# Kernel tuning notes

Hardware: AMD Instinct MI355X
Metric: run time of the kernel (lower is better)

## Reference

```python
import jax, jax.numpy as jnp
import numpy as np

B, S, H, NH = 2, 2048, 1024, 16
HD = H // NH


def setup_inputs() -> dict:
    key = jax.random.key(0)
    ks = jax.random.split(key, 12)
    query = jax.random.normal(ks[0], (B, S, H), dtype=jnp.float32)
    key_t = jax.random.normal(ks[1], (B, S, H), dtype=jnp.float32)
    value = jax.random.normal(ks[2], (B, S, H), dtype=jnp.float32)
    kpm = jax.random.randint(ks[3], (B, S), 0, 2).astype(bool)
    kpm = kpm.at[:, 0].set(False)  # guarantee at least one unmasked key per row
    bias = jax.random.normal(ks[4], (1, NH, S, S), dtype=jnp.float32)
    init = 0.02
    q_w = jax.random.normal(ks[5], (H, H), dtype=jnp.float32) * init
    k_w = jax.random.normal(ks[6], (H, H), dtype=jnp.float32) * init
    v_w = jax.random.normal(ks[7], (H, H), dtype=jnp.float32) * init
    o_w = jax.random.normal(ks[8], (H, H), dtype=jnp.float32) * init
    q_b = jnp.zeros((H,), jnp.float32)
    k_b = jnp.zeros((H,), jnp.float32)
    v_b = jnp.zeros((H,), jnp.float32)
    o_b = jnp.zeros((H,), jnp.float32)
    return {"query": query, "key": key_t, "value": value,
            "key_padding_mask": kpm, "bias": bias,
            "q_w": q_w, "q_b": q_b, "k_w": k_w, "k_b": k_b,
            "v_w": v_w, "v_b": v_b, "o_w": o_w, "o_b": o_b}


def _shape(x):
    # [B, S, H] -> [B, NH, S, HD]
    b, s, _ = x.shape
    return x.reshape(b, s, NH, HD).transpose(0, 2, 1, 3)


def reference(query, key, value, key_padding_mask, bias,
              q_w, q_b, k_w, k_b, v_w, v_b, o_w, o_b):
    scale = HD ** -0.5
    q = _shape(query @ q_w.T + q_b)
    k = _shape(key @ k_w.T + k_b)
    v = _shape(value @ v_w.T + v_b)
    attn = jnp.einsum('bhqd,bhkd->bhqk', q, k) * scale + bias
    mask = key_padding_mask[:, None, None, :]  # [B,1,1,S]
    attn = jnp.where(mask, -jnp.inf, attn)
    probs = jax.nn.softmax(attn, axis=-1)
    # safe-softmax: zero masked entries and renormalize with clamped denom
    probs = jnp.where(mask, 0.0, probs)
    denom = jnp.maximum(probs.sum(axis=-1, keepdims=True), 1e-6)
    probs = probs / denom
    ctx = jnp.einsum('bhqk,bhkd->bhqd', probs, v)
    ctx = ctx.transpose(0, 2, 1, 3).reshape(query.shape[0], query.shape[1], H)
    return ctx @ o_w.T + o_b
```

## Files before the change

### kernel.cpp

```cpp
#include <hip/hip_runtime.h>
#include <math.h>

#define Ss  2048
#define Hh  1024

typedef unsigned short u16;
typedef __attribute__((ext_vector_type(8))) short short8;
typedef __attribute__((ext_vector_type(4))) float fx4;

__device__ __forceinline__ u16 f2bf(float f) {
  unsigned int u = __float_as_uint(f);
  u = (u + 0x7fffu + ((u >> 16) & 1u)) >> 16;
  return (u16)u;
}

__device__ __forceinline__ void gld_lds16(const u16* g, u16* l) {
  __builtin_amdgcn_global_load_lds(
      (const __attribute__((address_space(1))) unsigned int*)(const unsigned int*)g,
      (__attribute__((address_space(3))) unsigned int*)(unsigned int*)l, 16, 0, 0);
}

#define MFMA16(a,b,c) __builtin_amdgcn_mfma_f32_16x16x32_bf16((a),(b),(c),0,0,0)

__global__ __launch_bounds__(256) void cast3(const float* __restrict__ a,
    const float* __restrict__ b, const float* __restrict__ c,
    u16* __restrict__ oa, u16* __restrict__ ob, u16* __restrict__ oc) {
  const int z = blockIdx.z;
  const float* in = z == 0 ? a : (z == 1 ? b : c);
  u16* out = z == 0 ? oa : (z == 1 ? ob : oc);
  const int i = (blockIdx.x * 256 + threadIdx.x) * 4;
  const float4 v = *(const float4*)(in + i);
  ushort4 r; r.x = f2bf(v.x); r.y = f2bf(v.y); r.z = f2bf(v.z); r.w = f2bf(v.w);
  *(ushort4*)(out + i) = r;
}

__global__ __launch_bounds__(256) void cast4(const float* __restrict__ a,
    const float* __restrict__ b, const float* __restrict__ c, const float* __restrict__ d,
    u16* __restrict__ oa, u16* __restrict__ ob, u16* __restrict__ oc, u16* __restrict__ od) {
  const int z = blockIdx.z;
  const float* in = z == 0 ? a : (z == 1 ? b : (z == 2 ? c : d));
  u16* out = z == 0 ? oa : (z == 1 ? ob : (z == 2 ? oc : od));
  const int i = (blockIdx.x * 256 + threadIdx.x) * 4;
  const float4 v = *(const float4*)(in + i);
  ushort4 r; r.x = f2bf(v.x); r.y = f2bf(v.y); r.z = f2bf(v.z); r.w = f2bf(v.w);
  *(ushort4*)(out + i) = r;
}

__global__ __launch_bounds__(256) void build_maskadd(const int* __restrict__ kpm,
                                                     float* __restrict__ ma) {
  const int i = blockIdx.x * 256 + threadIdx.x;
  ma[i] = kpm[i] ? -1.0e30f : 0.0f;
}

template <int MODE>
__device__ __forceinline__ void gemm_core(const u16* __restrict__ A,
    const u16* __restrict__ W, const float* __restrict__ bias,
    void* __restrict__ out, float scale) {
  __shared__ __align__(16) u16 As[2][4096];
  __shared__ __align__(16) u16 Bs[2][4096];
  const int tid = threadIdx.x;
  const int w = tid >> 6, lane = tid & 63, ln = lane & 15, quad = lane >> 4;
  const int i0 = blockIdx.y * 128, j0 = blockIdx.x * 128;
  const int wr = (w & 1) * 64, wc = (w >> 1) * 64;
  fx4 acc[4][4] = {};
  const int L0 = w * 64 + lane, L1 = L0 + 256;
  const u16* sa0 = A + (size_t)(i0 + (L0 & 127)) * 1024 + (L0 >> 7) * 8;
  const u16* sa1 = A + (size_t)(i0 + (L1 & 127)) * 1024 + (L1 >> 7) * 8;
  const u16* sb0 = W + (size_t)(j0 + (L0 & 127)) * 1024 + (L0 >> 7) * 8;
  const u16* sb1 = W + (size_t)(j0 + (L1 & 127)) * 1024 + (L1 >> 7) * 8;
  const int d0 = (w * 64) * 8, d1 = (256 + w * 64) * 8;

  gld_lds16(sa0, &As[0][d0]); gld_lds16(sa1, &As[0][d1]);
  gld_lds16(sb0, &Bs[0][d0]); gld_lds16(sb1, &Bs[0][d1]);
  __syncthreads();

  for (int k0 = 0; k0 < 1024; k0 += 32) {
    const int cur = (k0 >> 5) & 1;
    if (k0 + 32 < 1024) {
      const int nb = cur ^ 1;
      gld_lds16(sa0 + k0 + 32, &As[nb][d0]); gld_lds16(sa1 + k0 + 32, &As[nb][d1]);
      gld_lds16(sb0 + k0 + 32, &Bs[nb][d0]); gld_lds16(sb1 + k0 + 32, &Bs[nb][d1]);
    }
    short8 a[4], b[4];
#pragma unroll
    for (int t = 0; t < 4; ++t) {
      a[t] = *(const short8*)&As[cur][(quad * 128 + wr + t * 16 + ln) * 8];
      b[t] = *(const short8*)&Bs[cur][(quad * 128 + wc + t * 16 + ln) * 8];
    }
#pragma unroll
    for (int mt = 0; mt < 4; ++mt)
#pragma unroll
      for (int nt = 0; nt < 4; ++nt)
        acc[mt][nt] = MFMA16(a[mt], b[nt], acc[mt][nt]);
    __syncthreads();
  }
#pragma unroll
  for (int nt = 0; nt < 4; ++nt) {
    const int col = j0 + wc + nt * 16 + ln;
    const float bv = bias[col];
#pragma unroll
    for (int mt = 0; mt < 4; ++mt)
#pragma unroll
      for (int r = 0; r < 4; ++r) {
        const int row = i0 + wr + mt * 16 + quad * 4 + r;
        const float val = (acc[mt][nt][r] + bv) * scale;
        if (MODE == 1) {
          const int bb = row >> 11, s = row & 2047, h = col >> 6, d = col & 63;
          ((u16*)out)[((size_t)(bb * 16 + h) * 2048 + s) * 64 + d] = f2bf(val);
        } else {
          ((float*)out)[(size_t)row * 1024 + col] = val;
        }
      }
  }
}

__global__ __launch_bounds__(256) void gemm_qkv(
    const u16* xq, const u16* xk, const u16* xv,
    const u16* wq, const u16* wk, const u16* wv,
    const float* bq, const float* bk, const float* bv,
    u16* q, u16* k, u16* v) {
  const int z = blockIdx.z;
  const u16* A = z == 0 ? xq : (z == 1 ? xk : xv);
  const u16* W = z == 0 ? wq : (z == 1 ? wk : wv);
  const float* bb = z == 0 ? bq : (z == 1 ? bk : bv);
  u16* o = z == 0 ? q : (z == 1 ? k : v);
  const float sc = z == 0 ? 0.125f : 1.0f;
  gemm_core<1>(A, W, bb, o, sc);
}

__global__ __launch_bounds__(256) void gemm_o(const u16* ctx, const u16* wo,
                                              const float* ob, float* out) {
  gemm_core<0>(ctx, wo, ob, out, 1.0f);
}

__global__ __launch_bounds__(256) void transpose_v(const u16* __restrict__ v,
                                                   u16* __restrict__ vt) {
  __shared__ u16 T[64][72];
  const int tid = threadIdx.x;
  const int bh = blockIdx.y, s0 = blockIdx.x * 64;
#pragma unroll
  for (int i = 0; i < 2; ++i) {
    const int L = i * 256 + tid, key = L >> 3, dc = L & 7;
    const uint4 val = *(const uint4*)&v[((size_t)bh * 2048 + s0 + key) * 64 + dc * 8];
    *(uint4*)&T[key][dc * 8] = val;
  }
  __syncthreads();
#pragma unroll
  for (int i = 0; i < 2; ++i) {
    const int L = i * 256 + tid, d = L >> 3, kc = L & 7;
    u16 tmp[8];
#pragma unroll
    for (int j = 0; j < 8; ++j) tmp[j] = T[kc * 8 + j][d];
    *(uint4*)&vt[((size_t)bh * 64 + d) * 2048 + s0 + kc * 8] = *(const uint4*)tmp;
  }
}

__global__ __launch_bounds__(256) void attn(const u16* __restrict__ Qb,
    const u16* __restrict__ Kb, const u16* __restrict__ VT,
    const float* __restrict__ bias, const float* __restrict__ maskadd,
    u16* __restrict__ ctx) {
  __shared__ __align__(16) u16 Ks[2][4096];
  __shared__ __align__(16) u16 Vs[2][4096];
  __shared__ __align__(16) u16 Ps[4096];
  const int tid = threadIdx.x;
  const int w = tid >> 6, lane = tid & 63, ln = lane & 15, quad = lane >> 4;
  const int q0 = blockIdx.x * 64;
  const int hb = blockIdx.y, h = hb >> 1, b = hb & 1, bh = b * 16 + h;
  const int wr = w * 16;

  short8 qf[2];
#pragma unroll
  for (int ks = 0; ks < 2; ++ks)
    qf[ks] = *(const short8*)&Qb[((size_t)bh * 2048 + q0 + wr + ln) * 64 +
                                 ks * 32 + quad * 8];
  float mi[4], li[4];
  fx4 O[4] = {};
#pragma unroll
  for (int r = 0; r < 4; ++r) { mi[r] = -3.0e38f; li[r] = 0.f; }

  const int L0 = w * 64 + lane, L1 = L0 + 256;
  const u16* sk0 = Kb + ((size_t)bh * 2048 + (L0 & 63)) * 64 + (L0 >> 6) * 8;
  const u16* sk1 = Kb + ((size_t)bh * 2048 + (L1 & 63)) * 64 + (L1 >> 6) * 8;
  const u16* sv0 = VT + ((size_t)bh * 64 + (L0 & 63)) * 2048 + (L0 >> 6) * 8;
  const u16* sv1 = VT + ((size_t)bh * 64 + (L1 & 63)) * 2048 + (L1 >> 6) * 8;
  const int d0 = (w * 64) * 8, d1 = (256 + w * 64) * 8;

  const float* bq = bias + (size_t)h * Ss * Ss;

  gld_lds16(sk0, &Ks[0][d0]); gld_lds16(sk1, &Ks[0][d1]);
  gld_lds16(sv0, &Vs[0][d0]); gld_lds16(sv1, &Vs[0][d1]);
  float bcur[4][4], macur[4];
#pragma unroll
  for (int r = 0; r < 4; ++r) {
    const int qg = q0 + wr + quad * 4 + r;
#pragma unroll
    for (int nt = 0; nt < 4; ++nt)
      bcur[nt][r] = bq[(size_t)qg * Ss + nt * 16 + ln];
  }
#pragma unroll
  for (int nt = 0; nt < 4; ++nt) macur[nt] = maskadd[b * Ss + nt * 16 + ln];
  __syncthreads();

  for (int kt = 0; kt < Ss; kt += 64) {
    const int cur = (kt >> 6) & 1;
    if (kt + 64 < Ss) {
      const int nb = cur ^ 1;
      gld_lds16(sk0 + (size_t)(kt + 64) * 64, &Ks[nb][d0]);
      gld_lds16(sk1 + (size_t)(kt + 64) * 64, &Ks[nb][d1]);
      gld_lds16(sv0 + kt + 64, &Vs[nb][d0]);
      gld_lds16(sv1 + kt + 64, &Vs[nb][d1]);
    }
    const int kn = (kt + 64 < Ss) ? kt + 64 : kt;
    float bnxt[4][4], manxt[4];
#pragma unroll
    for (int r = 0; r < 4; ++r) {
      const int qg = q0 + wr + quad * 4 + r;
#pragma unroll
      for (int nt = 0; nt < 4; ++nt)
        bnxt[nt][r] = bq[(size_t)qg * Ss + kn + nt * 16 + ln];
    }
#pragma unroll
    for (int nt = 0; nt < 4; ++nt) manxt[nt] = maskadd[b * Ss + kn + nt * 16 + ln];

    fx4 S[4] = {};
#pragma unroll
    for (int ks = 0; ks < 2; ++ks)
#pragma unroll
      for (int nt = 0; nt < 4; ++nt) {
        const short8 kf = *(const short8*)&Ks[cur][((ks * 4 + quad) * 64 + nt * 16 + ln) * 8];
        S[nt] = MFMA16(qf[ks], kf, S[nt]);
      }

    float alpha[4];
#pragma unroll
    for (int r = 0; r < 4; ++r) {
      const float s0 = S[0][r] + bcur[0][r] + macur[0];
      const float s1 = S[1][r] + bcur[1][r] + macur[1];
      const float s2 = S[2][r] + bcur[2][r] + macur[2];
      const float s3 = S[3][r] + bcur[3][r] + macur[3];
      float mx = fmaxf(fmaxf(s0, s1), fmaxf(s2, s3));
      mx = fmaxf(mx, __shfl_xor(mx, 1)); mx = fmaxf(mx, __shfl_xor(mx, 2));
      mx = fmaxf(mx, __shfl_xor(mx, 4)); mx = fmaxf(mx, __shfl_xor(mx, 8));
      const float mn = fmaxf(mi[r], mx);
      const float a = __expf(mi[r] - mn);
      const float p0 = __expf(s0 - mn), p1 = __expf(s1 - mn);
      const float p2 = __expf(s2 - mn), p3 = __expf(s3 - mn);
      float rs = p0 + p1 + p2 + p3;
      rs += __shfl_xor(rs, 1); rs += __shfl_xor(rs, 2);
      rs += __shfl_xor(rs, 4); rs += __shfl_xor(rs, 8);
      li[r] = li[r] * a + rs;
      mi[r] = mn; alpha[r] = a;
      const int q = wr + quad * 4 + r;
      const int kcb = ln >> 3, jj = ln & 7;
      Ps[((kcb    ) * 64 + q) * 8 + jj] = f2bf(p0);
      Ps[((kcb + 2) * 64 + q) * 8 + jj] = f2bf(p1);
      Ps[((kcb + 4) * 64 + q) * 8 + jj] = f2bf(p2);
      Ps[((kcb + 6) * 64 + q) * 8 + jj] = f2bf(p3);
    }

#pragma unroll
    for (int nt = 0; nt < 4; ++nt)
#pragma unroll
      for (int r = 0; r < 4; ++r) O[nt][r] *= alpha[r];

#pragma unroll
    for (int ks = 0; ks < 2; ++ks) {
      const short8 pf = *(const short8*)&Ps[((ks * 4 + quad) * 64 + wr + ln) * 8];
#pragma unroll
      for (int nt = 0; nt < 4; ++nt) {
        const short8 vf = *(const short8*)&Vs[cur][((ks * 4 + quad) * 64 + nt * 16 + ln) * 8];
        O[nt] = MFMA16(pf, vf, O[nt]);
      }
    }

#pragma unroll
    for (int r = 0; r < 4; ++r) {
      macur[r] = manxt[r];
#pragma unroll
      for (int nt = 0; nt < 4; ++nt) bcur[nt][r] = bnxt[nt][r];
    }
    __syncthreads();
  }

#pragma unroll
  for (int r = 0; r < 4; ++r) {
    const float inv = 1.0f / fmaxf(li[r], 1e-6f);
    const int qg = q0 + wr + quad * 4 + r;
#pragma unroll
    for (int nt = 0; nt < 4; ++nt)
      ctx[((size_t)(b * Ss + qg)) * 1024 + h * 64 + nt * 16 + ln] =
          f2bf(O[nt][r] * inv);
  }
}

extern "C" void kernel_launch(void* const* d_in, const int* in_sizes, int n_in,
                              void* d_out, int out_size, void* d_ws, size_t ws_size,
                              hipStream_t stream) {
  const float* query = (const float*)d_in[0];
  const float* key   = (const float*)d_in[1];
  const float* value = (const float*)d_in[2];
  const int*   kpm   = (const int*)d_in[3];
  const float* bias  = (const float*)d_in[4];
  const float* q_w   = (const float*)d_in[5];
  const float* q_b   = (const float*)d_in[6];
  const float* k_w   = (const float*)d_in[7];
  const float* k_b   = (const float*)d_in[8];
  const float* v_w   = (const float*)d_in[9];
  const float* v_b   = (const float*)d_in[10];
  const float* o_w   = (const float*)d_in[11];
  const float* o_b   = (const float*)d_in[12];
  float* out = (float*)d_out;

  char* ws = (char*)d_ws;
  const size_t MB = 1024 * 1024;
  u16* xq = (u16*)(ws + 0 * MB);
  u16* xk = (u16*)(ws + 8 * MB);
  u16* xv = (u16*)(ws + 16 * MB);
  u16* wq = (u16*)(ws + 24 * MB);
  u16* wk = (u16*)(ws + 26 * MB);
  u16* wv = (u16*)(ws + 28 * MB);
  u16* wo = (u16*)(ws + 30 * MB);
  u16* qb = (u16*)(ws + 32 * MB);
  u16* kb = (u16*)(ws + 40 * MB);
  u16* vb = (u16*)(ws + 48 * MB);
  u16* cx = (u16*)(ws + 56 * MB);
  u16* vt = (u16*)(ws + 0 * MB);
  float* ma = (float*)(ws + 8 * MB);

  cast3<<<dim3(4096, 1, 3), 256, 0, stream>>>(query, key, value, xq, xk, xv);
  cast4<<<dim3(1024, 1, 4), 256, 0, stream>>>(q_w, k_w, v_w, o_w, wq, wk, wv, wo);
  gemm_qkv<<<dim3(8, 32, 3), 256, 0, stream>>>(xq, xk, xv, wq, wk, wv,
                                               q_b, k_b, v_b, qb, kb, vb);
  transpose_v<<<dim3(32, 32), 256, 0, stream>>>(vb, vt);
  build_maskadd<<<dim3(16), 256, 0, stream>>>(kpm, ma);
  attn<<<dim3(32, 32), 256, 0, stream>>>(qb, kb, vt, bias, ma, cx);
  gemm_o<<<dim3(8, 32), 256, 0, stream>>>(cx, wo, o_b, out);
}
```

Baseline: 611.2 us.

## Transpose QK^T MFMA so each lane owns a query row; lazy rescale softmax

Swaps the MFMA operands so S is computed transposed and each lane holds one query row's scores. Row max and row sum then need only two cross-lane shuffles instead of four per row. Bias and mask are loaded as float4 vectors and pre-summed. The online-softmax rescale of O is skipped unless some row's max grows by more than 8, and P is packed to bf16 with v_cvt_pk_bf16_f32 and stored as 8-byte LDS writes. This cuts shuffle, exp and scalar-store overhead in the inner loop. In exchange, skipping the rescale lets exp values reach e^8 before being stored as bf16, and O gains extra per-row shuffles when a rescale does happen.

```diff
diff --git a/kernel.cpp b/kernel.cpp
--- a/kernel.cpp
+++ b/kernel.cpp
@@ -173,10 +173,8 @@
   for (int ks = 0; ks < 2; ++ks)
     qf[ks] = *(const short8*)&Qb[((size_t)bh * 2048 + q0 + wr + ln) * 64 +
                                  ks * 32 + quad * 8];
-  float mi[4], li[4];
+  float mi = -3.0e38f, li = 0.f;
   fx4 O[4] = {};
-#pragma unroll
-  for (int r = 0; r < 4; ++r) { mi[r] = -3.0e38f; li[r] = 0.f; }
 
   const int L0 = w * 64 + lane, L1 = L0 + 256;
   const u16* sk0 = Kb + ((size_t)bh * 2048 + (L0 & 63)) * 64 + (L0 >> 6) * 8;
@@ -185,20 +183,19 @@
   const u16* sv1 = VT + ((size_t)bh * 64 + (L1 & 63)) * 2048 + (L1 >> 6) * 8;
   const int d0 = (w * 64) * 8, d1 = (256 + w * 64) * 8;
 
-  const float* bq = bias + (size_t)h * Ss * Ss;
+  const float* bp = bias + (size_t)h * Ss * Ss + (size_t)(q0 + wr + ln) * Ss + quad * 4;
+  const float* mp = maskadd + b * Ss + quad * 4;
 
   gld_lds16(sk0, &Ks[0][d0]); gld_lds16(sk1, &Ks[0][d1]);
   gld_lds16(sv0, &Vs[0][d0]); gld_lds16(sv1, &Vs[0][d1]);
-  float bcur[4][4], macur[4];
-#pragma unroll
-  for (int r = 0; r < 4; ++r) {
-    const int qg = q0 + wr + quad * 4 + r;
-#pragma unroll
-    for (int nt = 0; nt < 4; ++nt)
-      bcur[nt][r] = bq[(size_t)qg * Ss + nt * 16 + ln];
-  }
-#pragma unroll
-  for (int nt = 0; nt < 4; ++nt) macur[nt] = maskadd[b * Ss + nt * 16 + ln];
+  fx4 bm[4];
+#pragma unroll
+  for (int nt = 0; nt < 4; ++nt) {
+    const float4 bv = *(const float4*)(bp + nt * 16);
+    const float4 mv = *(const float4*)(mp + nt * 16);
+    bm[nt][0] = bv.x + mv.x; bm[nt][1] = bv.y + mv.y;
+    bm[nt][2] = bv.z + mv.z; bm[nt][3] = bv.w + mv.w;
+  }
   __syncthreads();
 
   for (int kt = 0; kt < Ss; kt += 64) {
@@ -211,16 +208,14 @@
       gld_lds16(sv1 + kt + 64, &Vs[nb][d1]);
     }
     const int kn = (kt + 64 < Ss) ? kt + 64 : kt;
-    float bnxt[4][4], manxt[4];
-#pragma unroll
-    for (int r = 0; r < 4; ++r) {
-      const int qg = q0 + wr + quad * 4 + r;
-#pragma unroll
-      for (int nt = 0; nt < 4; ++nt)
-        bnxt[nt][r] = bq[(size_t)qg * Ss + kn + nt * 16 + ln];
-    }
-#pragma unroll
-    for (int nt = 0; nt < 4; ++nt) manxt[nt] = maskadd[b * Ss + kn + nt * 16 + ln];
+    fx4 bmn[4];
+#pragma unroll
+    for (int nt = 0; nt < 4; ++nt) {
+      const float4 bv = *(const float4*)(bp + kn + nt * 16);
+      const float4 mv = *(const float4*)(mp + kn + nt * 16);
+      bmn[nt][0] = bv.x + mv.x; bmn[nt][1] = bv.y + mv.y;
+      bmn[nt][2] = bv.z + mv.z; bmn[nt][3] = bv.w + mv.w;
+    }
 
     fx4 S[4] = {};
 #pragma unroll
@@ -228,40 +223,54 @@
 #pragma unroll
       for (int nt = 0; nt < 4; ++nt) {
         const short8 kf = *(const short8*)&Ks[cur][((ks * 4 + quad) * 64 + nt * 16 + ln) * 8];
-        S[nt] = MFMA16(qf[ks], kf, S[nt]);
-      }
-
-    float alpha[4];
-#pragma unroll
-    for (int r = 0; r < 4; ++r) {
-      const float s0 = S[0][r] + bcur[0][r] + macur[0];
-      const float s1 = S[1][r] + bcur[1][r] + macur[1];
-      const float s2 = S[2][r] + bcur[2][r] + macur[2];
-      const float s3 = S[3][r] + bcur[3][r] + macur[3];
-      float mx = fmaxf(fmaxf(s0, s1), fmaxf(s2, s3));
-      mx = fmaxf(mx, __shfl_xor(mx, 1)); mx = fmaxf(mx, __shfl_xor(mx, 2));
-      mx = fmaxf(mx, __shfl_xor(mx, 4)); mx = fmaxf(mx, __shfl_xor(mx, 8));
-      const float mn = fmaxf(mi[r], mx);
-      const float a = __expf(mi[r] - mn);
-      const float p0 = __expf(s0 - mn), p1 = __expf(s1 - mn);
-      const float p2 = __expf(s2 - mn), p3 = __expf(s3 - mn);
-      float rs = p0 + p1 + p2 + p3;
-      rs += __shfl_xor(rs, 1); rs += __shfl_xor(rs, 2);
-      rs += __shfl_xor(rs, 4); rs += __shfl_xor(rs, 8);
-      li[r] = li[r] * a + rs;
-      mi[r] = mn; alpha[r] = a;
-      const int q = wr + quad * 4 + r;
-      const int kcb = ln >> 3, jj = ln & 7;
-      Ps[((kcb    ) * 64 + q) * 8 + jj] = f2bf(p0);
-      Ps[((kcb + 2) * 64 + q) * 8 + jj] = f2bf(p1);
-      Ps[((kcb + 4) * 64 + q) * 8 + jj] = f2bf(p2);
-      Ps[((kcb + 6) * 64 + q) * 8 + jj] = f2bf(p3);
-    }
-
+        S[nt] = MFMA16(kf, qf[ks], S[nt]);
+      }
+
+    float pmax = -3.0e38f;
 #pragma unroll
     for (int nt = 0; nt < 4; ++nt)
 #pragma unroll
-      for (int r = 0; r < 4; ++r) O[nt][r] *= alpha[r];
+      for (int r = 0; r < 4; ++r) {
+        S[nt][r] += bm[nt][r];
+        pmax = fmaxf(pmax, S[nt][r]);
+      }
+    pmax = fmaxf(pmax, __shfl_xor(pmax, 16));
+    pmax = fmaxf(pmax, __shfl_xor(pmax, 32));
+
+    if (!__all(pmax <= mi + 8.0f)) {
+      const float mn = fmaxf(mi, pmax);
+      const float a = __expf(mi - mn);
+#pragma unroll
+      for (int r = 0; r < 4; ++r) {
+        const float ar = __shfl(a, quad * 4 + r);
+#pragma unroll
+        for (int nt = 0; nt < 4; ++nt) O[nt][r] *= ar;
+      }
+      li *= a;
+      mi = mn;
+    }
+
+    float rs = 0.f;
+#pragma unroll
+    for (int nt = 0; nt < 4; ++nt)
+#pragma unroll
+      for (int r = 0; r < 4; ++r) {
+        S[nt][r] = __expf(S[nt][r] - mi);
+        rs += S[nt][r];
+      }
+    rs += __shfl_xor(rs, 16);
+    rs += __shfl_xor(rs, 32);
+    li += rs;
+
+#pragma unroll
+    for (int nt = 0; nt < 4; ++nt) {
+      unsigned int u0, u1;
+      asm("v_cvt_pk_bf16_f32 %0, %1, %2" : "=v"(u0) : "v"(S[nt][0]), "v"(S[nt][1]));
+      asm("v_cvt_pk_bf16_f32 %0, %1, %2" : "=v"(u1) : "v"(S[nt][2]), "v"(S[nt][3]));
+      const int kcb = nt * 2 + (quad >> 1);
+      uint2 pk; pk.x = u0; pk.y = u1;
+      *(uint2*)&Ps[(kcb * 64 + wr + ln) * 8 + (quad & 1) * 4] = pk;
+    }
 
 #pragma unroll
     for (int ks = 0; ks < 2; ++ks) {
@@ -274,17 +283,14 @@
     }
 
 #pragma unroll
-    for (int r = 0; r < 4; ++r) {
-      macur[r] = manxt[r];
-#pragma unroll
-      for (int nt = 0; nt < 4; ++nt) bcur[nt][r] = bnxt[nt][r];
-    }
+    for (int nt = 0; nt < 4; ++nt) bm[nt] = bmn[nt];
     __syncthreads();
   }
 
 #pragma unroll
   for (int r = 0; r < 4; ++r) {
-    const float inv = 1.0f / fmaxf(li[r], 1e-6f);
+    const float lr = __shfl(li, quad * 4 + r);
+    const float inv = 1.0f / fmaxf(lr, 1e-6f);
     const int qg = q0 + wr + quad * 4 + r;
 #pragma unroll
     for (int nt = 0; nt < 4; ++nt)
```

After: 598.1 us. 1.02x faster.
